# Kernel optimization log

Hardware: AMD Instinct MI355X
Metric: run time of the kernel (lower is better)

## Reference

```python
import jax, jax.numpy as jnp
import numpy as np
from jax import lax

INPUT_SIZE = 24
HIDDEN = 64
LAYERS = 3
SEQ = 14
BATCH = 65536
CLASS_NUM = 10


def setup_inputs() -> dict:
    key = jax.random.key(0)
    ks = jax.random.split(key, 16)
    s_ih0 = 1.0 / np.sqrt(HIDDEN)
    inp = {
        'x': jax.random.normal(ks[0], (BATCH, SEQ, INPUT_SIZE), dtype=jnp.float32),
        'h0': jnp.zeros((LAYERS, BATCH, HIDDEN), dtype=jnp.float32),
        # layer 0
        'W_ih0': jax.random.uniform(ks[1], (HIDDEN, INPUT_SIZE), jnp.float32, -s_ih0, s_ih0),
        'W_hh0': jax.random.uniform(ks[2], (HIDDEN, HIDDEN), jnp.float32, -s_ih0, s_ih0),
        'b_ih0': jax.random.uniform(ks[3], (HIDDEN,), jnp.float32, -s_ih0, s_ih0),
        'b_hh0': jax.random.uniform(ks[4], (HIDDEN,), jnp.float32, -s_ih0, s_ih0),
        # layer 1
        'W_ih1': jax.random.uniform(ks[5], (HIDDEN, HIDDEN), jnp.float32, -s_ih0, s_ih0),
        'W_hh1': jax.random.uniform(ks[6], (HIDDEN, HIDDEN), jnp.float32, -s_ih0, s_ih0),
        'b_ih1': jax.random.uniform(ks[7], (HIDDEN,), jnp.float32, -s_ih0, s_ih0),
        'b_hh1': jax.random.uniform(ks[8], (HIDDEN,), jnp.float32, -s_ih0, s_ih0),
        # layer 2
        'W_ih2': jax.random.uniform(ks[9], (HIDDEN, HIDDEN), jnp.float32, -s_ih0, s_ih0),
        'W_hh2': jax.random.uniform(ks[10], (HIDDEN, HIDDEN), jnp.float32, -s_ih0, s_ih0),
        'b_ih2': jax.random.uniform(ks[11], (HIDDEN,), jnp.float32, -s_ih0, s_ih0),
        'b_hh2': jax.random.uniform(ks[12], (HIDDEN,), jnp.float32, -s_ih0, s_ih0),
        # output head
        'W_out': jax.random.uniform(ks[13], (CLASS_NUM, HIDDEN), jnp.float32, -s_ih0, s_ih0),
        'b_out': jax.random.uniform(ks[14], (CLASS_NUM,), jnp.float32, -s_ih0, s_ih0),
    }
    return inp


def _rnn_layer(xs, h0_l, W_ih, W_hh, b_ih, b_hh):
    # xs: [T, B, in]; h0_l: [B, H]. Elman tanh recurrence.
    def step(h, x_t):
        h_new = jnp.tanh(x_t @ W_ih.T + b_ih + h @ W_hh.T + b_hh)
        return h_new, h_new
    h_T, ys = lax.scan(step, h0_l, xs)
    return ys, h_T  # ys: [T, B, H]


def reference(x, h0, W_ih0, W_hh0, b_ih0, b_hh0, W_ih1, W_hh1, b_ih1, b_hh1,
              W_ih2, W_hh2, b_ih2, b_hh2, W_out, b_out):
    # x: [B, T, 24] (batch_first) -> time-major [T, B, 24]
    xs = jnp.swapaxes(x, 0, 1)
    layer_params = [
        (W_ih0, W_hh0, b_ih0, b_hh0),
        (W_ih1, W_hh1, b_ih1, b_hh1),
        (W_ih2, W_hh2, b_ih2, b_hh2),
    ]
    h_finals = []
    for l, (Wi, Wh, bi, bh) in enumerate(layer_params):
        xs, h_T = _rnn_layer(xs, h0[l], Wi, Wh, bi, bh)
        h_finals.append(h_T)
        # inter-layer dropout is identity in eval mode
    last = xs[-1]  # [B, H] == r_out[:, -1, :]
    out = last @ W_out.T + b_out  # [B, CLASS_NUM]
    h_state = jnp.stack(h_finals, axis=0)  # [LAYERS, B, H]
    return out, h_state
```

## Files before the change

kernel.cpp:

```cpp
#include <hip/hip_runtime.h>
#include <hip/hip_bf16.h>

#define SEQ 14
#define IN 24
#define H 64
#define CLS 10
#define NBATCH 65536
#define NB 32
#define WSCALE 2.8853900817779268f

typedef __attribute__((ext_vector_type(4))) float f32x4;
typedef __attribute__((ext_vector_type(8))) short bf16x8;
typedef __attribute__((ext_vector_type(4))) short bf16x4;

#define MFMA(A, B, C) __builtin_amdgcn_mfma_f32_16x16x32_bf16(A, B, C, 0, 0, 0)
#define PIN(v) asm volatile("" : "+v"(v))

static __device__ __forceinline__ float fexp2(float x) {
#if __has_builtin(__builtin_amdgcn_exp2f)
    return __builtin_amdgcn_exp2f(x);
#else
    return __expf(x * 0.6931471805599453f);
#endif
}
static __device__ __forceinline__ float tanh2(float y) {
    float e = fexp2(y);
    return fmaf(-2.0f, __builtin_amdgcn_rcpf(e + 1.0f), 1.0f);
}
static __device__ __forceinline__ short f2bf(float f) {
    __hip_bfloat16 h = __float2bfloat16(f);
    union { __hip_bfloat16 h; short s; } u; u.h = h;
    return u.s;
}
static __device__ __forceinline__ bf16x8 pack8(f32x4 a, f32x4 b) {
    bf16x8 r;
    r[0] = f2bf(a[0]); r[1] = f2bf(a[1]); r[2] = f2bf(a[2]); r[3] = f2bf(a[3]);
    r[4] = f2bf(b[0]); r[5] = f2bf(b[1]); r[6] = f2bf(b[2]); r[7] = f2bf(b[3]);
    return r;
}
static __device__ __forceinline__ bf16x8 loadw8(const float* p) {
    return pack8(*(const f32x4*)p, *(const f32x4*)(p + 4));
}
static __device__ __forceinline__ bf16x8 loadw8s(const float* p, float s) {
    f32x4 a = *(const f32x4*)p, b = *(const f32x4*)(p + 4);
    return pack8(a * s, b * s);
}

__global__ __launch_bounds__(256, 2) void rnn_mfma(
    const float* __restrict__ x,
    const float* __restrict__ h0in,
    const float* __restrict__ pWi0, const float* __restrict__ pWh0,
    const float* __restrict__ pbi0, const float* __restrict__ pbh0,
    const float* __restrict__ pWi1, const float* __restrict__ pWh1,
    const float* __restrict__ pbi1, const float* __restrict__ pbh1,
    const float* __restrict__ pWi2, const float* __restrict__ pWh2,
    const float* __restrict__ pbi2, const float* __restrict__ pbh2,
    const float* __restrict__ pWout, const float* __restrict__ pbout,
    float* __restrict__ out)
{
    __shared__ __align__(16) short hbuf[2][3][8][NB][8];

    const int tid  = threadIdx.x;
    const int lane = tid & 63;
    const int g    = lane >> 4;
    const int c    = lane & 15;
    const int mt   = tid >> 6;
    const int b0   = blockIdx.x * NB;

    {
        const int b = tid & 31, k8 = (tid >> 5) & 7;
#pragma unroll
        for (int l = 0; l < 3; ++l) {
            const float* p = h0in + ((size_t)l * NBATCH + (b0 + b)) * H + k8 * 8;
            *(bf16x8*)&hbuf[(l + 1) & 1][l][k8][b][0] =
                pack8(*(const f32x4*)p, *(const f32x4*)(p + 4));
        }
    }

    const int ia = mt * 16 + c;
    bf16x8 aWi0;
    if (g < 3) aWi0 = loadw8s(pWi0 + ia * IN + g * 8, WSCALE);
    else {
#pragma unroll
        for (int j = 0; j < 8; ++j) aWi0[j] = 0;
    }
    PIN(aWi0);
    bf16x8 aWh0[2], aWi1[2], aWh1[2], aWi2[2], aWh2[2];
#pragma unroll
    for (int kt = 0; kt < 2; ++kt) {
        aWh0[kt] = loadw8s(pWh0 + ia * H + kt * 32 + g * 8, WSCALE);  PIN(aWh0[kt]);
        aWi1[kt] = loadw8s(pWi1 + ia * H + kt * 32 + g * 8, WSCALE);  PIN(aWi1[kt]);
        aWh1[kt] = loadw8s(pWh1 + ia * H + kt * 32 + g * 8, WSCALE);  PIN(aWh1[kt]);
        aWi2[kt] = loadw8s(pWi2 + ia * H + kt * 32 + g * 8, WSCALE);  PIN(aWi2[kt]);
        aWh2[kt] = loadw8s(pWh2 + ia * H + kt * 32 + g * 8, WSCALE);  PIN(aWh2[kt]);
    }

    const int i0 = mt * 16 + g * 4;
    f32x4 bs0 = (*(const f32x4*)(pbi0 + i0) + *(const f32x4*)(pbh0 + i0)) * WSCALE;
    f32x4 bs1 = (*(const f32x4*)(pbi1 + i0) + *(const f32x4*)(pbh1 + i0)) * WSCALE;
    f32x4 bs2 = (*(const f32x4*)(pbi2 + i0) + *(const f32x4*)(pbh2 + i0)) * WSCALE;
    PIN(bs0); PIN(bs1); PIN(bs2);

    const int kgw = mt * 2 + (g >> 1);
    const int eb  = (g & 1) * 4;

    const float* xb0 = x + (size_t)(b0 + c) * (SEQ * IN) + g * 8;
    const float* xb1 = x + (size_t)(b0 + 16 + c) * (SEQ * IN) + g * 8;
    float* hsout = out + (size_t)NBATCH * CLS;

    __syncthreads();

#define L0S(s_)                                                                 \
    {                                                                           \
        const int pr = ((s_) + 1) & 1, pw = (s_) & 1, t = (s_);                 \
        bf16x8 bx0, bx1;                                                        \
        _Pragma("unroll")                                                       \
        for (int j = 0; j < 8; ++j) { bx0[j] = 0; bx1[j] = 0; }                 \
        if (g < 3) {                                                            \
            const float* p0 = xb0 + t * IN;                                     \
            const float* p1 = xb1 + t * IN;                                     \
            bx0 = pack8(*(const f32x4*)p0, *(const f32x4*)(p0 + 4));            \
            bx1 = pack8(*(const f32x4*)p1, *(const f32x4*)(p1 + 4));            \
        }                                                                       \
        bf16x8 s0a = *(const bf16x8*)&hbuf[pr][0][g][c][0];                     \
        bf16x8 s0b = *(const bf16x8*)&hbuf[pr][0][g][c + 16][0];                \
        bf16x8 s1a = *(const bf16x8*)&hbuf[pr][0][4 + g][c][0];                 \
        bf16x8 s1b = *(const bf16x8*)&hbuf[pr][0][4 + g][c + 16][0];            \
        f32x4 a0 = bs0, a1 = bs0;                                               \
        a0 = MFMA(aWh0[0], s0a, a0);  a1 = MFMA(aWh0[0], s0b, a1);              \
        a0 = MFMA(aWh0[1], s1a, a0);  a1 = MFMA(aWh0[1], s1b, a1);              \
        a0 = MFMA(aWi0,    bx0, a0);  a1 = MFMA(aWi0,    bx1, a1);              \
        f32x4 t0, t1;                                                           \
        _Pragma("unroll")                                                       \
        for (int r = 0; r < 4; ++r) { t0[r] = tanh2(a0[r]); t1[r] = tanh2(a1[r]); } \
        if (t == SEQ - 1) {                                                     \
            *(f32x4*)(hsout + (size_t)(b0 + c) * H + i0) = t0;                  \
            *(f32x4*)(hsout + (size_t)(b0 + 16 + c) * H + i0) = t1;             \
        }                                                                       \
        bf16x4 p0v, p1v;                                                        \
        _Pragma("unroll")                                                       \
        for (int r = 0; r < 4; ++r) { p0v[r] = f2bf(t0[r]); p1v[r] = f2bf(t1[r]); } \
        *(bf16x4*)&hbuf[pw][0][kgw][c][eb] = p0v;                               \
        *(bf16x4*)&hbuf[pw][0][kgw][c + 16][eb] = p1v;                          \
    }

#define L12S(s_, li, bsv, aWhX, aWiX)                                           \
    {                                                                           \
        const int pr = ((s_) + 1) & 1, pw = (s_) & 1, t = (s_) - (li);          \
        bf16x8 s0a = *(const bf16x8*)&hbuf[pr][li][g][c][0];                    \
        bf16x8 s0b = *(const bf16x8*)&hbuf[pr][li][g][c + 16][0];               \
        bf16x8 s1a = *(const bf16x8*)&hbuf[pr][li][4 + g][c][0];                \
        bf16x8 s1b = *(const bf16x8*)&hbuf[pr][li][4 + g][c + 16][0];           \
        bf16x8 b0a = *(const bf16x8*)&hbuf[pr][li - 1][g][c][0];                \
        bf16x8 b0b = *(const bf16x8*)&hbuf[pr][li - 1][g][c + 16][0];           \
        bf16x8 b1a = *(const bf16x8*)&hbuf[pr][li - 1][4 + g][c][0];            \
        bf16x8 b1b = *(const bf16x8*)&hbuf[pr][li - 1][4 + g][c + 16][0];       \
        f32x4 a0 = bsv, a1 = bsv;                                               \
        a0 = MFMA(aWhX[0], s0a, a0);  a1 = MFMA(aWhX[0], s0b, a1);              \
        a0 = MFMA(aWhX[1], s1a, a0);  a1 = MFMA(aWhX[1], s1b, a1);              \
        a0 = MFMA(aWiX[0], b0a, a0);  a1 = MFMA(aWiX[0], b0b, a1);              \
        a0 = MFMA(aWiX[1], b1a, a0);  a1 = MFMA(aWiX[1], b1b, a1);              \
        f32x4 t0, t1;                                                           \
        _Pragma("unroll")                                                       \
        for (int r = 0; r < 4; ++r) { t0[r] = tanh2(a0[r]); t1[r] = tanh2(a1[r]); } \
        if (t == SEQ - 1) {                                                     \
            float* hp = hsout + (size_t)(li) * NBATCH * H;                      \
            *(f32x4*)(hp + (size_t)(b0 + c) * H + i0) = t0;                     \
            *(f32x4*)(hp + (size_t)(b0 + 16 + c) * H + i0) = t1;                \
        }                                                                       \
        bf16x4 p0v, p1v;                                                        \
        _Pragma("unroll")                                                       \
        for (int r = 0; r < 4; ++r) { p0v[r] = f2bf(t0[r]); p1v[r] = f2bf(t1[r]); } \
        *(bf16x4*)&hbuf[pw][li][kgw][c][eb] = p0v;                              \
        *(bf16x4*)&hbuf[pw][li][kgw][c + 16][eb] = p1v;                         \
    }

    L0S(0);
    __syncthreads();
    L0S(1);
    L12S(1, 1, bs1, aWh1, aWi1);
    __syncthreads();

#pragma unroll 1
    for (int s = 2; s < SEQ; ++s) {
        L0S(s);
        L12S(s, 1, bs1, aWh1, aWi1);
        L12S(s, 2, bs2, aWh2, aWi2);
        __syncthreads();
    }

    L12S(SEQ, 1, bs1, aWh1, aWi1);
    L12S(SEQ, 2, bs2, aWh2, aWi2);
    __syncthreads();
    L12S(SEQ + 1, 2, bs2, aWh2, aWi2);
    __syncthreads();

#undef L0S
#undef L12S

    if (mt < 2) {
        bf16x8 aWo0, aWo1;
#pragma unroll
        for (int j = 0; j < 8; ++j) { aWo0[j] = 0; aWo1[j] = 0; }
        if (c < CLS) {
            aWo0 = loadw8(pWout + c * H + 8 * g);
            aWo1 = loadw8(pWout + c * H + 32 + 8 * g);
        }
        const int col = c + 16 * mt;
        bf16x8 s0 = *(const bf16x8*)&hbuf[1][2][g][col][0];
        bf16x8 s1 = *(const bf16x8*)&hbuf[1][2][4 + g][col][0];
        f32x4 acc = {0.f, 0.f, 0.f, 0.f};
        acc = MFMA(aWo0, s0, acc);
        acc = MFMA(aWo1, s1, acc);
#pragma unroll
        for (int r = 0; r < 4; ++r) {
            const int cls = 4 * g + r;
            if (cls < CLS)
                out[(size_t)(b0 + col) * CLS + cls] = acc[r] + pbout[cls];
        }
    }
}

extern "C" void kernel_launch(void* const* d_in, const int* in_sizes, int n_in,
                              void* d_out, int out_size, void* d_ws, size_t ws_size,
                              hipStream_t stream) {
    const float* x    = (const float*)d_in[0];
    const float* h0in = (const float*)d_in[1];
    const float* Wi0  = (const float*)d_in[2];
    const float* Wh0  = (const float*)d_in[3];
    const float* bi0  = (const float*)d_in[4];
    const float* bh0  = (const float*)d_in[5];
    const float* Wi1  = (const float*)d_in[6];
    const float* Wh1  = (const float*)d_in[7];
    const float* bi1  = (const float*)d_in[8];
    const float* bh1  = (const float*)d_in[9];
    const float* Wi2  = (const float*)d_in[10];
    const float* Wh2  = (const float*)d_in[11];
    const float* bi2  = (const float*)d_in[12];
    const float* bh2  = (const float*)d_in[13];
    const float* Wout = (const float*)d_in[14];
    const float* bout = (const float*)d_in[15];
    float* out = (float*)d_out;

    dim3 grid(NBATCH / NB), block(256);
    rnn_mfma<<<grid, block, 0, stream>>>(x, h0in, Wi0, Wh0, bi0, bh0,
                                         Wi1, Wh1, bi1, bh1,
                                         Wi2, Wh2, bi2, bh2,
                                         Wout, bout, out);
}
```

Before: 92.10 us.

## Split warp tiles 2x2 over hidden rows and batch columns

Each of the four waves now owns two 16-row hidden tiles and one 16-column batch tile, where before it owned one 16-row hidden tile across both batch halves. The weight fragments each wave keeps in registers double, and the number of LDS reads of the hidden state per wave halves. The x load per step also halves. The trade is much higher register pressure from the doubled pinned weights, which could hurt occupancy at launch bounds of 256 threads and 2 blocks per SM.

```diff
diff --git a/kernel.cpp b/kernel.cpp
--- a/kernel.cpp
+++ b/kernel.cpp
@@ -64,7 +64,10 @@
     const int lane = tid & 63;
     const int g    = lane >> 4;
     const int c    = lane & 15;
-    const int mt   = tid >> 6;
+    const int wid  = tid >> 6;
+    const int mi   = wid >> 1;
+    const int ni   = wid & 1;
+    const int cc   = c + 16 * ni;
     const int b0   = blockIdx.x * NB;
 
     {
@@ -77,35 +80,38 @@
         }
     }
 
-    const int ia = mt * 16 + c;
-    bf16x8 aWi0;
-    if (g < 3) aWi0 = loadw8s(pWi0 + ia * IN + g * 8, WSCALE);
-    else {
-#pragma unroll
-        for (int j = 0; j < 8; ++j) aWi0[j] = 0;
-    }
-    PIN(aWi0);
-    bf16x8 aWh0[2], aWi1[2], aWh1[2], aWi2[2], aWh2[2];
-#pragma unroll
-    for (int kt = 0; kt < 2; ++kt) {
-        aWh0[kt] = loadw8s(pWh0 + ia * H + kt * 32 + g * 8, WSCALE);  PIN(aWh0[kt]);
-        aWi1[kt] = loadw8s(pWi1 + ia * H + kt * 32 + g * 8, WSCALE);  PIN(aWi1[kt]);
-        aWh1[kt] = loadw8s(pWh1 + ia * H + kt * 32 + g * 8, WSCALE);  PIN(aWh1[kt]);
-        aWi2[kt] = loadw8s(pWi2 + ia * H + kt * 32 + g * 8, WSCALE);  PIN(aWi2[kt]);
-        aWh2[kt] = loadw8s(pWh2 + ia * H + kt * 32 + g * 8, WSCALE);  PIN(aWh2[kt]);
-    }
-
-    const int i0 = mt * 16 + g * 4;
-    f32x4 bs0 = (*(const f32x4*)(pbi0 + i0) + *(const f32x4*)(pbh0 + i0)) * WSCALE;
-    f32x4 bs1 = (*(const f32x4*)(pbi1 + i0) + *(const f32x4*)(pbh1 + i0)) * WSCALE;
-    f32x4 bs2 = (*(const f32x4*)(pbi2 + i0) + *(const f32x4*)(pbh2 + i0)) * WSCALE;
-    PIN(bs0); PIN(bs1); PIN(bs2);
-
-    const int kgw = mt * 2 + (g >> 1);
-    const int eb  = (g & 1) * 4;
-
-    const float* xb0 = x + (size_t)(b0 + c) * (SEQ * IN) + g * 8;
-    const float* xb1 = x + (size_t)(b0 + 16 + c) * (SEQ * IN) + g * 8;
+    bf16x8 aWh0[2][2], aWi1[2][2], aWh1[2][2], aWi2[2][2], aWh2[2][2], aWi0[2];
+#pragma unroll
+    for (int mtl = 0; mtl < 2; ++mtl) {
+        const int row = 32 * mi + 16 * mtl + c;
+#pragma unroll
+        for (int kt = 0; kt < 2; ++kt) {
+            aWh0[mtl][kt] = loadw8s(pWh0 + row * H + kt * 32 + g * 8, WSCALE); PIN(aWh0[mtl][kt]);
+            aWi1[mtl][kt] = loadw8s(pWi1 + row * H + kt * 32 + g * 8, WSCALE); PIN(aWi1[mtl][kt]);
+            aWh1[mtl][kt] = loadw8s(pWh1 + row * H + kt * 32 + g * 8, WSCALE); PIN(aWh1[mtl][kt]);
+            aWi2[mtl][kt] = loadw8s(pWi2 + row * H + kt * 32 + g * 8, WSCALE); PIN(aWi2[mtl][kt]);
+            aWh2[mtl][kt] = loadw8s(pWh2 + row * H + kt * 32 + g * 8, WSCALE); PIN(aWh2[mtl][kt]);
+        }
+        if (g < 3) aWi0[mtl] = loadw8s(pWi0 + row * IN + g * 8, WSCALE);
+        else {
+#pragma unroll
+            for (int j = 0; j < 8; ++j) aWi0[mtl][j] = 0;
+        }
+        PIN(aWi0[mtl]);
+    }
+
+    f32x4 bs0[2], bs1[2], bs2[2];
+#pragma unroll
+    for (int mtl = 0; mtl < 2; ++mtl) {
+        const int i0 = 32 * mi + 16 * mtl + 4 * g;
+        bs0[mtl] = (*(const f32x4*)(pbi0 + i0) + *(const f32x4*)(pbh0 + i0)) * WSCALE;
+        bs1[mtl] = (*(const f32x4*)(pbi1 + i0) + *(const f32x4*)(pbh1 + i0)) * WSCALE;
+        bs2[mtl] = (*(const f32x4*)(pbi2 + i0) + *(const f32x4*)(pbh2 + i0)) * WSCALE;
+        PIN(bs0[mtl]); PIN(bs1[mtl]); PIN(bs2[mtl]);
+    }
+
+    const int eb = (g & 1) * 4;
+    const float* xb = x + (size_t)(b0 + cc) * (SEQ * IN) + g * 8;
     float* hsout = out + (size_t)NBATCH * CLS;
 
     __syncthreads();
@@ -113,66 +119,60 @@
 #define L0S(s_)                                                                 \
     {                                                                           \
         const int pr = ((s_) + 1) & 1, pw = (s_) & 1, t = (s_);                 \
-        bf16x8 bx0, bx1;                                                        \
+        bf16x8 xB;                                                              \
         _Pragma("unroll")                                                       \
-        for (int j = 0; j < 8; ++j) { bx0[j] = 0; bx1[j] = 0; }                 \
+        for (int j = 0; j < 8; ++j) xB[j] = 0;                                  \
         if (g < 3) {                                                            \
-            const float* p0 = xb0 + t * IN;                                     \
-            const float* p1 = xb1 + t * IN;                                     \
-            bx0 = pack8(*(const f32x4*)p0, *(const f32x4*)(p0 + 4));            \
-            bx1 = pack8(*(const f32x4*)p1, *(const f32x4*)(p1 + 4));            \
+            const float* xp = xb + t * IN;                                      \
+            xB = pack8(*(const f32x4*)xp, *(const f32x4*)(xp + 4));             \
         }                                                                       \
-        bf16x8 s0a = *(const bf16x8*)&hbuf[pr][0][g][c][0];                     \
-        bf16x8 s0b = *(const bf16x8*)&hbuf[pr][0][g][c + 16][0];                \
-        bf16x8 s1a = *(const bf16x8*)&hbuf[pr][0][4 + g][c][0];                 \
-        bf16x8 s1b = *(const bf16x8*)&hbuf[pr][0][4 + g][c + 16][0];            \
-        f32x4 a0 = bs0, a1 = bs0;                                               \
-        a0 = MFMA(aWh0[0], s0a, a0);  a1 = MFMA(aWh0[0], s0b, a1);              \
-        a0 = MFMA(aWh0[1], s1a, a0);  a1 = MFMA(aWh0[1], s1b, a1);              \
-        a0 = MFMA(aWi0,    bx0, a0);  a1 = MFMA(aWi0,    bx1, a1);              \
-        f32x4 t0, t1;                                                           \
+        bf16x8 s0 = *(const bf16x8*)&hbuf[pr][0][g][cc][0];                     \
+        bf16x8 s1 = *(const bf16x8*)&hbuf[pr][0][4 + g][cc][0];                 \
         _Pragma("unroll")                                                       \
-        for (int r = 0; r < 4; ++r) { t0[r] = tanh2(a0[r]); t1[r] = tanh2(a1[r]); } \
-        if (t == SEQ - 1) {                                                     \
-            *(f32x4*)(hsout + (size_t)(b0 + c) * H + i0) = t0;                  \
-            *(f32x4*)(hsout + (size_t)(b0 + 16 + c) * H + i0) = t1;             \
+        for (int mtl = 0; mtl < 2; ++mtl) {                                     \
+            f32x4 acc = bs0[mtl];                                               \
+            acc = MFMA(aWh0[mtl][0], s0, acc);                                  \
+            acc = MFMA(aWh0[mtl][1], s1, acc);                                  \
+            acc = MFMA(aWi0[mtl], xB, acc);                                     \
+            f32x4 th;                                                           \
+            _Pragma("unroll")                                                   \
+            for (int r = 0; r < 4; ++r) th[r] = tanh2(acc[r]);                  \
+            if (t == SEQ - 1)                                                   \
+                *(f32x4*)(hsout + (size_t)(b0 + cc) * H +                       \
+                          32 * mi + 16 * mtl + 4 * g) = th;                     \
+            bf16x4 pv;                                                          \
+            _Pragma("unroll")                                                   \
+            for (int r = 0; r < 4; ++r) pv[r] = f2bf(th[r]);                    \
+            *(bf16x4*)&hbuf[pw][0][4 * mi + 2 * mtl + (g >> 1)][cc][eb] = pv;   \
         }                                                                       \
-        bf16x4 p0v, p1v;                                                        \
-        _Pragma("unroll")                                                       \
-        for (int r = 0; r < 4; ++r) { p0v[r] = f2bf(t0[r]); p1v[r] = f2bf(t1[r]); } \
-        *(bf16x4*)&hbuf[pw][0][kgw][c][eb] = p0v;                               \
-        *(bf16x4*)&hbuf[pw][0][kgw][c + 16][eb] = p1v;                          \
     }
 
 #define L12S(s_, li, bsv, aWhX, aWiX)                                           \
     {                                                                           \
         const int pr = ((s_) + 1) & 1, pw = (s_) & 1, t = (s_) - (li);          \
-        bf16x8 s0a = *(const bf16x8*)&hbuf[pr][li][g][c][0];                    \
-        bf16x8 s0b = *(const bf16x8*)&hbuf[pr][li][g][c + 16][0];               \
-        bf16x8 s1a = *(const bf16x8*)&hbuf[pr][li][4 + g][c][0];                \
-        bf16x8 s1b = *(const bf16x8*)&hbuf[pr][li][4 + g][c + 16][0];           \
-        bf16x8 b0a = *(const bf16x8*)&hbuf[pr][li - 1][g][c][0];                \
-        bf16x8 b0b = *(const bf16x8*)&hbuf[pr][li - 1][g][c + 16][0];           \
-        bf16x8 b1a = *(const bf16x8*)&hbuf[pr][li - 1][4 + g][c][0];            \
-        bf16x8 b1b = *(const bf16x8*)&hbuf[pr][li - 1][4 + g][c + 16][0];       \
-        f32x4 a0 = bsv, a1 = bsv;                                               \
-        a0 = MFMA(aWhX[0], s0a, a0);  a1 = MFMA(aWhX[0], s0b, a1);              \
-        a0 = MFMA(aWhX[1], s1a, a0);  a1 = MFMA(aWhX[1], s1b, a1);              \
-        a0 = MFMA(aWiX[0], b0a, a0);  a1 = MFMA(aWiX[0], b0b, a1);              \
-        a0 = MFMA(aWiX[1], b1a, a0);  a1 = MFMA(aWiX[1], b1b, a1);              \
-        f32x4 t0, t1;                                                           \
+        bf16x8 s0 = *(const bf16x8*)&hbuf[pr][li][g][cc][0];                    \
+        bf16x8 s1 = *(const bf16x8*)&hbuf[pr][li][4 + g][cc][0];                \
+        bf16x8 u0 = *(const bf16x8*)&hbuf[pr][li - 1][g][cc][0];                \
+        bf16x8 u1 = *(const bf16x8*)&hbuf[pr][li - 1][4 + g][cc][0];            \
         _Pragma("unroll")                                                       \
-        for (int r = 0; r < 4; ++r) { t0[r] = tanh2(a0[r]); t1[r] = tanh2(a1[r]); } \
-        if (t == SEQ - 1) {                                                     \
-            float* hp = hsout + (size_t)(li) * NBATCH * H;                      \
-            *(f32x4*)(hp + (size_t)(b0 + c) * H + i0) = t0;                     \
-            *(f32x4*)(hp + (size_t)(b0 + 16 + c) * H + i0) = t1;                \
+        for (int mtl = 0; mtl < 2; ++mtl) {                                     \
+            f32x4 acc = bsv[mtl];                                               \
+            acc = MFMA(aWhX[mtl][0], s0, acc);                                  \
+            acc = MFMA(aWhX[mtl][1], s1, acc);                                  \
+            acc = MFMA(aWiX[mtl][0], u0, acc);                                  \
+            acc = MFMA(aWiX[mtl][1], u1, acc);                                  \
+            f32x4 th;                                                           \
+            _Pragma("unroll")                                                   \
+            for (int r = 0; r < 4; ++r) th[r] = tanh2(acc[r]);                  \
+            if (t == SEQ - 1)                                                   \
+                *(f32x4*)(hsout + (size_t)(li) * NBATCH * H +                   \
+                          (size_t)(b0 + cc) * H +                               \
+                          32 * mi + 16 * mtl + 4 * g) = th;                     \
+            bf16x4 pv;                                                          \
+            _Pragma("unroll")                                                   \
+            for (int r = 0; r < 4; ++r) pv[r] = f2bf(th[r]);                    \
+            *(bf16x4*)&hbuf[pw][li][4 * mi + 2 * mtl + (g >> 1)][cc][eb] = pv;  \
         }                                                                       \
-        bf16x4 p0v, p1v;                                                        \
-        _Pragma("unroll")                                                       \
-        for (int r = 0; r < 4; ++r) { p0v[r] = f2bf(t0[r]); p1v[r] = f2bf(t1[r]); } \
-        *(bf16x4*)&hbuf[pw][li][kgw][c][eb] = p0v;                              \
-        *(bf16x4*)&hbuf[pw][li][kgw][c + 16][eb] = p1v;                         \
     }
 
     L0S(0);
@@ -198,7 +198,7 @@
 #undef L0S
 #undef L12S
 
-    if (mt < 2) {
+    if (mi == 0) {
         bf16x8 aWo0, aWo1;
 #pragma unroll
         for (int j = 0; j < 8; ++j) { aWo0[j] = 0; aWo1[j] = 0; }
@@ -206,9 +206,8 @@
             aWo0 = loadw8(pWout + c * H + 8 * g);
             aWo1 = loadw8(pWout + c * H + 32 + 8 * g);
         }
-        const int col = c + 16 * mt;
-        bf16x8 s0 = *(const bf16x8*)&hbuf[1][2][g][col][0];
-        bf16x8 s1 = *(const bf16x8*)&hbuf[1][2][4 + g][col][0];
+        bf16x8 s0 = *(const bf16x8*)&hbuf[1][2][g][cc][0];
+        bf16x8 s1 = *(const bf16x8*)&hbuf[1][2][4 + g][cc][0];
         f32x4 acc = {0.f, 0.f, 0.f, 0.f};
         acc = MFMA(aWo0, s0, acc);
         acc = MFMA(aWo1, s1, acc);
@@ -216,7 +215,7 @@
         for (int r = 0; r < 4; ++r) {
             const int cls = 4 * g + r;
             if (cls < CLS)
-                out[(size_t)(b0 + col) * CLS + cls] = acc[r] + pbout[cls];
+                out[(size_t)(b0 + cc) * CLS + cls] = acc[r] + pbout[cls];
         }
     }
 }
```

After: 107.4 us. 16.6% more time.
